# Kernel tuning notes

Measured on AMD Instinct MI355X. Metric: run time of the kernel, lower is better.

Reference implementation:

```python
import jax, jax.numpy as jnp
import numpy as np

EMBED = 1024
HEADS = 16
HEAD_DIM = EMBED // HEADS


def setup_inputs() -> dict:
    key = jax.random.key(0)
    ks = jax.random.split(key, 6)
    s = 1.0 / np.sqrt(EMBED)
    return {
        "x": jax.random.normal(ks[0], (2, 2048, EMBED), dtype=jnp.float32),
        "Wq": jax.random.normal(ks[1], (EMBED, EMBED), dtype=jnp.float32) * s,
        "Wk": jax.random.normal(ks[2], (EMBED, EMBED), dtype=jnp.float32) * s,
        "Wv": jax.random.normal(ks[3], (EMBED, EMBED), dtype=jnp.float32) * s,
        "Wfc": jax.random.normal(ks[4], (EMBED, EMBED), dtype=jnp.float32) * s,
        "bfc": jnp.zeros((EMBED,), dtype=jnp.float32),
    }


def reference(x, Wq, Wk, Wv, Wfc, bfc):
    # x: (N, L, E). Linear(E,E,bias=False) applies y = x @ W.T (torch convention).
    N, L, E = x.shape
    q = (x @ Wq.T).reshape(N, L, HEADS, HEAD_DIM)
    k = (x @ Wk.T).reshape(N, L, HEADS, HEAD_DIM)
    v = (x @ Wv.T).reshape(N, L, HEADS, HEAD_DIM)
    # energy: (N, H, Q, K)
    energy = jnp.einsum('nqhd,nkhd->nhqk', q, k)
    # NOTE: original scales by sqrt(embed_size), not sqrt(head_dim)
    attn = jax.nn.softmax(energy / jnp.sqrt(jnp.float32(E)), axis=3)
    out = jnp.einsum('nhql,nlhd->nqhd', attn, v).reshape(N, L, E)
    return out @ Wfc.T + bfc
```

## Files before the change

kernel.cpp:

```cpp
#include <hip/hip_runtime.h>
#include <stdint.h>


typedef short bf16x8 __attribute__((ext_vector_type(8)));
typedef short bf16x4 __attribute__((ext_vector_type(4)));
typedef float f32x4 __attribute__((ext_vector_type(4)));

__device__ __forceinline__ unsigned short f2bf(float f) {
  union { float f; unsigned u; } v; v.f = f;
  return (unsigned short)((v.u + 0x7FFFu + ((v.u >> 16) & 1u)) >> 16);
}

#if defined(__has_builtin)
#if __has_builtin(__builtin_amdgcn_cvt_pk_bf16_f32)
#define HAVE_PK_BF16 1
#endif
#if __has_builtin(__builtin_amdgcn_exp2f)
#define EXP2(x) __builtin_amdgcn_exp2f(x)
#endif
#endif
#ifndef EXP2
#define EXP2(x) exp2f(x)
#endif

__device__ __forceinline__ unsigned pk2bf(float a, float b) {
#ifdef HAVE_PK_BF16
  typedef __bf16 bfv2 __attribute__((ext_vector_type(2)));
  union { bfv2 v; unsigned u; } c;
  c.v = __builtin_amdgcn_cvt_pk_bf16_f32(a, b);
  return c.u;
#else
  return (unsigned)f2bf(a) | ((unsigned)f2bf(b) << 16);
#endif
}

__device__ __forceinline__ void load_lds16(const unsigned short* g, unsigned short* l) {
  __builtin_amdgcn_global_load_lds(
      (const __attribute__((address_space(1))) unsigned int*)(const void*)g,
      (__attribute__((address_space(3))) unsigned int*)(void*)l, 16, 0, 0);
}

#define MFMA16(a, b, c) __builtin_amdgcn_mfma_f32_16x16x32_bf16((a), (b), (c), 0, 0, 0)

#if defined(__has_builtin)
#if __has_builtin(__builtin_amdgcn_mfma_f32_16x16x16bf16_1k)
#define MFMAK16(a, b, c) __builtin_amdgcn_mfma_f32_16x16x16bf16_1k((a), (b), (c), 0, 0, 0)
#elif __has_builtin(__builtin_amdgcn_mfma_f32_16x16x16_bf16)
#define MFMAK16(a, b, c) __builtin_amdgcn_mfma_f32_16x16x16_bf16((a), (b), (c), 0, 0, 0)
#endif
#endif
#ifndef MFMAK16
__device__ __forceinline__ f32x4 mfmak16_asm(bf16x4 a, bf16x4 b, f32x4 c) {
  asm volatile("v_mfma_f32_16x16x16_bf16 %0, %1, %2, %0" : "+v"(c) : "v"(a), "v"(b));
  return c;
}
#define MFMAK16(a, b, c) mfmak16_asm((a), (b), (c))
#endif

__global__ __launch_bounds__(256) void cvt_all_kernel(
    const float* __restrict__ x, const float* __restrict__ w0, const float* __restrict__ w1,
    const float* __restrict__ w2, const float* __restrict__ w3, unsigned short* __restrict__ xb,
    unsigned short* __restrict__ d0, unsigned short* __restrict__ d1,
    unsigned short* __restrict__ d2, unsigned short* __restrict__ d3) {
  int i = blockIdx.x * 256 + threadIdx.x;
  const float* s;
  unsigned short* d;
  int off;
  if (i < 1048576) {
    s = x; d = xb; off = i;
  } else {
    int j = i - 1048576;
    int w = j >> 18;
    off = j & 262143;
    s = (w == 0) ? w0 : (w == 1) ? w1 : (w == 2) ? w2 : w3;
    d = (w == 0) ? d0 : (w == 1) ? d1 : (w == 2) ? d2 : d3;
  }
  float4 f = ((const float4*)s)[off];
  uint2 o;
  o.x = pk2bf(f.x, f.y);
  o.y = pk2bf(f.z, f.w);
  ((uint2*)d)[off] = o;
}

__global__ __launch_bounds__(256) void gemm_qkv_kernel(
    const unsigned short* __restrict__ Xb, const unsigned short* __restrict__ Wqb,
    const unsigned short* __restrict__ Wkb, const unsigned short* __restrict__ Wvb,
    unsigned short* __restrict__ Qo, unsigned short* __restrict__ Ko,
    unsigned short* __restrict__ Vt) {
  __shared__ __align__(16) unsigned short As[128 * 32];
  __shared__ __align__(16) unsigned short Bs[128 * 32];
  const int mode = blockIdx.z;
  const unsigned short* W = (mode == 0) ? Wqb : ((mode == 1) ? Wkb : Wvb);
  const int n0 = blockIdx.x * 128;
  const int m0 = blockIdx.y * 128;
  const int tid = threadIdx.x;
  const int lane = tid & 63;
  const int wv = tid >> 6;
  const int wm = (wv >> 1) * 64;
  const int wn = (wv & 1) * 64;
  const int qq = lane >> 4;
  const int cc = lane & 15;

  const f32x4 fz = {0.f, 0.f, 0.f, 0.f};
  f32x4 acc[4][4];
#pragma unroll
  for (int i = 0; i < 4; i++)
#pragma unroll
    for (int j = 0; j < 4; j++) acc[i][j] = fz;

  const int ia0 = tid, ia1 = tid + 256;
  const int ra0 = ia0 >> 2, ca0 = (ia0 & 3) * 8;
  const int ra1 = ia1 >> 2, ca1 = (ia1 & 3) * 8;

  for (int k0 = 0; k0 < 1024; k0 += 32) {
    __syncthreads();
    load_lds16(Xb + (m0 + ra0) * 1024 + k0 + ca0, As + ia0 * 8);
    load_lds16(Xb + (m0 + ra1) * 1024 + k0 + ca1, As + ia1 * 8);
    load_lds16(W + (n0 + ra0) * 1024 + k0 + ca0, Bs + ia0 * 8);
    load_lds16(W + (n0 + ra1) * 1024 + k0 + ca1, Bs + ia1 * 8);
    __syncthreads();
    bf16x8 a[4], b[4];
#pragma unroll
    for (int i = 0; i < 4; i++) a[i] = *(const bf16x8*)(As + (wm + i * 16 + cc) * 32 + qq * 8);
#pragma unroll
    for (int j = 0; j < 4; j++) b[j] = *(const bf16x8*)(Bs + (wn + j * 16 + cc) * 32 + qq * 8);
    if (mode < 2) {
#pragma unroll
      for (int i = 0; i < 4; i++)
#pragma unroll
        for (int j = 0; j < 4; j++) acc[i][j] = MFMA16(b[j], a[i], acc[i][j]);
    } else {
#pragma unroll
      for (int i = 0; i < 4; i++)
#pragma unroll
        for (int j = 0; j < 4; j++) acc[i][j] = MFMA16(a[i], b[j], acc[i][j]);
    }
  }

  if (mode < 2) {
    const float esc = (mode == 0) ? 0.0450842200277801f : 1.0f;
    unsigned short* dst = (mode == 0) ? Qo : Ko;
#pragma unroll
    for (int i = 0; i < 4; i++) {
      int row = m0 + wm + i * 16 + cc;
#pragma unroll
      for (int j = 0; j < 4; j++) {
        int col = n0 + wn + j * 16 + qq * 4;
        uint2 pk;
        pk.x = pk2bf(acc[i][j][0] * esc, acc[i][j][1] * esc);
        pk.y = pk2bf(acc[i][j][2] * esc, acc[i][j][3] * esc);
        *(uint2*)(dst + row * 1024 + col) = pk;
      }
    }
  } else {
#pragma unroll
    for (int i = 0; i < 4; i++)
#pragma unroll
      for (int j = 0; j < 4; j++) {
        int row = m0 + wm + i * 16 + qq * 4;
        int nn = row >> 11, ll = row & 2047;
        int col = n0 + wn + j * 16 + cc;
        int hh = col >> 6, dd = col & 63;
        uint2 pk;
        pk.x = pk2bf(acc[i][j][0], acc[i][j][1]);
        pk.y = pk2bf(acc[i][j][2], acc[i][j][3]);
        *(uint2*)(Vt + ((nn * 16 + hh) * 64 + dd) * 2048 + ll) = pk;
      }
  }
}

__global__ __launch_bounds__(256, 2) void attn_kernel(const unsigned short* __restrict__ Qg,
                                                      const unsigned short* __restrict__ Kg,
                                                      const unsigned short* __restrict__ Vg,
                                                      unsigned short* __restrict__ Og) {
  __shared__ __align__(16) unsigned short smem[2][2][8192];
  const int qt = blockIdx.x, hh = blockIdx.y, nb = blockIdx.z;
  const int tid = threadIdx.x, lane = tid & 63, wv = tid >> 6;
  const int pair = wv >> 1, wq = wv & 1;
  const int qq = lane >> 4, cc = lane & 15;
  const int q0 = qt * 128 + wq * 64;
  const unsigned short* Kbase = Kg + (size_t)(nb * 2048 + pair * 1024) * 1024 + hh * 64;
  const unsigned short* Vbase = Vg + (size_t)((nb * 16 + hh) * 64) * 2048 + pair * 1024;

  const int lr = lane >> 3;
  const int lc8 = ((lane & 7) ^ lr) * 8;
  const int ldl = lane * 8;

  bf16x8 qf[4][2];
#pragma unroll
  for (int rt = 0; rt < 4; rt++)
#pragma unroll
    for (int kc = 0; kc < 2; kc++)
      qf[rt][kc] = *(const bf16x8*)(Qg + (size_t)(nb * 2048 + q0 + rt * 16 + cc) * 1024 +
                                    hh * 64 + kc * 32 + qq * 8);

  const f32x4 fz = {0.f, 0.f, 0.f, 0.f};
  f32x4 o[4][4];
  float lsum[4] = {0.f, 0.f, 0.f, 0.f};
#pragma unroll
  for (int rt = 0; rt < 4; rt++)
#pragma unroll
    for (int vt = 0; vt < 4; vt++) o[rt][vt] = fz;

  {
    unsigned short* Kb = &smem[pair][0][0];
    unsigned short* Vb = &smem[pair][0][4096];
#pragma unroll
    for (int i = 0; i < 4; i++) {
      int CI = wq * 4 + i;
      load_lds16(Kbase + (size_t)(CI * 8 + lr) * 1024 + lc8, Kb + CI * 512 + ldl);
      load_lds16(Vbase + (size_t)(CI * 8 + lr) * 2048 + lc8, Vb + CI * 512 + ldl);
    }
  }
  __syncthreads();

#pragma unroll 1
  for (int it = 0; it < 16; it++) {
    const int buf = it & 1;
    if (it < 15) {
      const int ktn = (it + 1) * 64;
      unsigned short* Kb = &smem[pair][buf ^ 1][0];
      unsigned short* Vb = &smem[pair][buf ^ 1][4096];
#pragma unroll
      for (int i = 0; i < 4; i++) {
        int CI = wq * 4 + i;
        load_lds16(Kbase + (size_t)(ktn + CI * 8 + lr) * 1024 + lc8, Kb + CI * 512 + ldl);
        load_lds16(Vbase + (size_t)(CI * 8 + lr) * 2048 + ktn + lc8, Vb + CI * 512 + ldl);
      }
    }
    const unsigned short* Kp = &smem[pair][buf][0];
    const unsigned short* Vp = &smem[pair][buf][4096];
#pragma unroll
    for (int st = 0; st < 4; st++) {
      const unsigned short* kr = Kp + (st * 16 + cc) * 64;
      int ch0 = (qq ^ (cc & 7)) << 3;
      bf16x8 k0 = *(const bf16x8*)(kr + ch0);
      bf16x8 k1 = *(const bf16x8*)(kr + (ch0 ^ 32));
      f32x4 z[4];
#pragma unroll
      for (int rt = 0; rt < 4; rt++) {
        z[rt] = MFMA16(k0, qf[rt][0], fz);
        z[rt] = MFMA16(k1, qf[rt][1], z[rt]);
      }
      bf16x4 bp[4];
#pragma unroll
      for (int rt = 0; rt < 4; rt++) {
        float p0 = EXP2(z[rt][0]), p1 = EXP2(z[rt][1]);
        float p2 = EXP2(z[rt][2]), p3 = EXP2(z[rt][3]);
        lsum[rt] += (p0 + p1) + (p2 + p3);
        union { uint2 u; bf16x4 v; } pk;
        pk.u.x = pk2bf(p0, p1);
        pk.u.y = pk2bf(p2, p3);
        bp[rt] = pk.v;
      }
      int vc = st * 2 + (qq >> 1);
      int voff = (qq & 1) * 4;
#pragma unroll
      for (int vt = 0; vt < 4; vt++) {
        bf16x4 vf = *(const bf16x4*)(Vp + (vt * 16 + cc) * 64 + ((vc ^ (cc & 7)) << 3) + voff);
#pragma unroll
        for (int rt = 0; rt < 4; rt++) o[rt][vt] = MFMAK16(vf, bp[rt], o[rt][vt]);
      }
    }
    __syncthreads();
  }

#pragma unroll
  for (int rt = 0; rt < 4; rt++) {
    float l = lsum[rt];
    l += __shfl_xor(l, 16);
    l += __shfl_xor(l, 32);
    lsum[rt] = l;
  }

  float* oex = (float*)&smem[0][0][0];
  float* lex = oex + 8192;
  __syncthreads();
  if (pair == 1) {
#pragma unroll
    for (int rt = 0; rt < 4; rt++) {
#pragma unroll
      for (int vt = 0; vt < 4; vt++) {
        int idx = (((wq * 4 + rt) * 4 + vt) * 4 + qq) * 16 + cc;
        *(f32x4*)(oex + idx * 4) = o[rt][vt];
      }
      if (qq == 0) lex[(wq * 4 + rt) * 16 + cc] = lsum[rt];
    }
  }
  __syncthreads();
  if (pair == 0) {
#pragma unroll
    for (int rt = 0; rt < 4; rt++) {
      float rinv = 1.0f / (lsum[rt] + lex[(wq * 4 + rt) * 16 + cc]);
#pragma unroll
      for (int vt = 0; vt < 4; vt++) {
        int idx = (((wq * 4 + rt) * 4 + vt) * 4 + qq) * 16 + cc;
        f32x4 op = *(const f32x4*)(oex + idx * 4);
        uint2 ov;
        ov.x = pk2bf((o[rt][vt][0] + op[0]) * rinv, (o[rt][vt][1] + op[1]) * rinv);
        ov.y = pk2bf((o[rt][vt][2] + op[2]) * rinv, (o[rt][vt][3] + op[3]) * rinv);
        *(uint2*)(Og + (size_t)(nb * 2048 + q0 + rt * 16 + cc) * 1024 + hh * 64 + vt * 16 +
                  qq * 4) = ov;
      }
    }
  }
}

__global__ __launch_bounds__(256) void gemm_fc_kernel(const unsigned short* __restrict__ Ab,
                                                      const unsigned short* __restrict__ Wb,
                                                      const float* __restrict__ bias,
                                                      float* __restrict__ Co) {
  __shared__ __align__(16) unsigned short As[64 * 32];
  __shared__ __align__(16) unsigned short Bs[128 * 32];
  const int n0 = blockIdx.x * 128;
  const int m0 = blockIdx.y * 64;
  const int tid = threadIdx.x;
  const int lane = tid & 63;
  const int wv = tid >> 6;
  const int wm = (wv & 1) * 32;
  const int wn = (wv >> 1) * 64;
  const int qq = lane >> 4;
  const int cc = lane & 15;

  const f32x4 fz = {0.f, 0.f, 0.f, 0.f};
  f32x4 acc[2][4];
#pragma unroll
  for (int i = 0; i < 2; i++)
#pragma unroll
    for (int j = 0; j < 4; j++) acc[i][j] = fz;

  const int raA = tid >> 2, caA = (tid & 3) * 8;
  const int ia0 = tid, ia1 = tid + 256;
  const int rb0 = ia0 >> 2, cb0 = (ia0 & 3) * 8;
  const int rb1 = ia1 >> 2, cb1 = (ia1 & 3) * 8;

  for (int k0 = 0; k0 < 1024; k0 += 32) {
    __syncthreads();
    load_lds16(Ab + (m0 + raA) * 1024 + k0 + caA, As + tid * 8);
    load_lds16(Wb + (n0 + rb0) * 1024 + k0 + cb0, Bs + ia0 * 8);
    load_lds16(Wb + (n0 + rb1) * 1024 + k0 + cb1, Bs + ia1 * 8);
    __syncthreads();
    bf16x8 a[2], b[4];
#pragma unroll
    for (int i = 0; i < 2; i++) a[i] = *(const bf16x8*)(As + (wm + i * 16 + cc) * 32 + qq * 8);
#pragma unroll
    for (int j = 0; j < 4; j++) b[j] = *(const bf16x8*)(Bs + (wn + j * 16 + cc) * 32 + qq * 8);
#pragma unroll
    for (int i = 0; i < 2; i++)
#pragma unroll
      for (int j = 0; j < 4; j++) acc[i][j] = MFMA16(b[j], a[i], acc[i][j]);
  }

#pragma unroll
  for (int i = 0; i < 2; i++) {
    int row = m0 + wm + i * 16 + cc;
#pragma unroll
    for (int j = 0; j < 4; j++) {
      int col = n0 + wn + j * 16 + qq * 4;
      float4 bb = *(const float4*)(bias + col);
      float4 ov;
      ov.x = acc[i][j][0] + bb.x;
      ov.y = acc[i][j][1] + bb.y;
      ov.z = acc[i][j][2] + bb.z;
      ov.w = acc[i][j][3] + bb.w;
      *(float4*)(Co + (size_t)row * 1024 + col) = ov;
    }
  }
}

extern "C" void kernel_launch(void* const* d_in, const int* in_sizes, int n_in, void* d_out,
                              int out_size, void* d_ws, size_t ws_size, hipStream_t stream) {
  const float* x = (const float*)d_in[0];
  const float* Wq = (const float*)d_in[1];
  const float* Wk = (const float*)d_in[2];
  const float* Wv = (const float*)d_in[3];
  const float* Wfc = (const float*)d_in[4];
  const float* bfc = (const float*)d_in[5];
  float* out = (float*)d_out;
  char* ws = (char*)d_ws;
  unsigned short* xb = (unsigned short*)(ws);
  unsigned short* wqb = (unsigned short*)(ws + (8u << 20));
  unsigned short* wkb = (unsigned short*)(ws + (10u << 20));
  unsigned short* wvb = (unsigned short*)(ws + (12u << 20));
  unsigned short* wfb = (unsigned short*)(ws + (14u << 20));
  unsigned short* Qb = (unsigned short*)(ws + (16u << 20));
  unsigned short* Kb = (unsigned short*)(ws + (24u << 20));
  unsigned short* Vtb = (unsigned short*)(ws + (32u << 20));
  unsigned short* Ob = (unsigned short*)(ws + (40u << 20));

  cvt_all_kernel<<<8192, 256, 0, stream>>>(x, Wq, Wk, Wv, Wfc, xb, wqb, wkb, wvb, wfb);
  gemm_qkv_kernel<<<dim3(8, 32, 3), 256, 0, stream>>>(xb, wqb, wkb, wvb, Qb, Kb, Vtb);
  attn_kernel<<<dim3(16, 16, 2), 256, 0, stream>>>(Qb, Kb, Vtb, Ob);
  gemm_fc_kernel<<<dim3(8, 64), 256, 0, stream>>>(Ob, wfb, bfc, out);
}
```

Baseline: 200.8 us.

## Double-buffer QKV GEMM LDS tiles with K=64 steps and XOR swizzle

Restructures the QKV projection GEMM main loop to use two LDS buffers with a K-step of 64. The next tile's global-to-LDS loads are issued before computing on the current one, leaving one barrier per iteration instead of two. It also XOR-swizzles the LDS column slots to reduce bank conflicts on the 16-byte fragment reads, and adds a launch bound hint of 2 blocks per CU. LDS use grows to 64KB per block, which may limit occupancy.

```diff
diff --git a/kernel.cpp b/kernel.cpp
--- a/kernel.cpp
+++ b/kernel.cpp
@@ -82,13 +82,12 @@
   ((uint2*)d)[off] = o;
 }
 
-__global__ __launch_bounds__(256) void gemm_qkv_kernel(
+__global__ __launch_bounds__(256, 2) void gemm_qkv_kernel(
     const unsigned short* __restrict__ Xb, const unsigned short* __restrict__ Wqb,
     const unsigned short* __restrict__ Wkb, const unsigned short* __restrict__ Wvb,
     unsigned short* __restrict__ Qo, unsigned short* __restrict__ Ko,
     unsigned short* __restrict__ Vt) {
-  __shared__ __align__(16) unsigned short As[128 * 32];
-  __shared__ __align__(16) unsigned short Bs[128 * 32];
+  __shared__ __align__(16) unsigned short smem[2][16384];
   const int mode = blockIdx.z;
   const unsigned short* W = (mode == 0) ? Wqb : ((mode == 1) ? Wkb : Wvb);
   const int n0 = blockIdx.x * 128;
@@ -108,33 +107,69 @@
 #pragma unroll
     for (int j = 0; j < 4; j++) acc[i][j] = fz;
 
-  const int ia0 = tid, ia1 = tid + 256;
-  const int ra0 = ia0 >> 2, ca0 = (ia0 & 3) * 8;
-  const int ra1 = ia1 >> 2, ca1 = (ia1 & 3) * 8;
-
-  for (int k0 = 0; k0 < 1024; k0 += 32) {
+  const int srow = tid >> 3;
+  const int scol = (((tid & 7) ^ (srow & 7)) * 8);
+  const unsigned short* gA[4];
+  const unsigned short* gB[4];
+#pragma unroll
+  for (int i = 0; i < 4; i++) {
+    gA[i] = Xb + (size_t)(m0 + i * 32 + srow) * 1024 + scol;
+    gB[i] = W + (size_t)(n0 + i * 32 + srow) * 1024 + scol;
+  }
+  const int ldst = tid * 8;
+
+#pragma unroll
+  for (int i = 0; i < 4; i++) {
+    load_lds16(gA[i], smem[0] + i * 2048 + ldst);
+    load_lds16(gB[i], smem[0] + 8192 + i * 2048 + ldst);
+    gA[i] += 64;
+    gB[i] += 64;
+  }
+  __syncthreads();
+
+#pragma unroll 1
+  for (int it = 0; it < 16; it++) {
+    const int buf = it & 1;
+    if (it < 15) {
+      unsigned short* dst = smem[buf ^ 1];
+#pragma unroll
+      for (int i = 0; i < 4; i++) {
+        load_lds16(gA[i], dst + i * 2048 + ldst);
+        load_lds16(gB[i], dst + 8192 + i * 2048 + ldst);
+        gA[i] += 64;
+        gB[i] += 64;
+      }
+    }
+    const unsigned short* Ab = smem[buf];
+    const unsigned short* Bb = smem[buf] + 8192;
+#pragma unroll
+    for (int kc = 0; kc < 2; kc++) {
+      bf16x8 a[4], b[4];
+#pragma unroll
+      for (int i = 0; i < 4; i++) {
+        int row = wm + i * 16 + cc;
+        int slot = (kc * 4 + qq) ^ (cc & 7);
+        a[i] = *(const bf16x8*)(Ab + row * 64 + slot * 8);
+      }
+#pragma unroll
+      for (int j = 0; j < 4; j++) {
+        int row = wn + j * 16 + cc;
+        int slot = (kc * 4 + qq) ^ (cc & 7);
+        b[j] = *(const bf16x8*)(Bb + row * 64 + slot * 8);
+      }
+      if (mode < 2) {
+#pragma unroll
+        for (int i = 0; i < 4; i++)
+#pragma unroll
+          for (int j = 0; j < 4; j++) acc[i][j] = MFMA16(b[j], a[i], acc[i][j]);
+      } else {
+#pragma unroll
+        for (int i = 0; i < 4; i++)
+#pragma unroll
+          for (int j = 0; j < 4; j++) acc[i][j] = MFMA16(a[i], b[j], acc[i][j]);
+      }
+    }
     __syncthreads();
-    load_lds16(Xb + (m0 + ra0) * 1024 + k0 + ca0, As + ia0 * 8);
-    load_lds16(Xb + (m0 + ra1) * 1024 + k0 + ca1, As + ia1 * 8);
-    load_lds16(W + (n0 + ra0) * 1024 + k0 + ca0, Bs + ia0 * 8);
-    load_lds16(W + (n0 + ra1) * 1024 + k0 + ca1, Bs + ia1 * 8);
-    __syncthreads();
-    bf16x8 a[4], b[4];
-#pragma unroll
-    for (int i = 0; i < 4; i++) a[i] = *(const bf16x8*)(As + (wm + i * 16 + cc) * 32 + qq * 8);
-#pragma unroll
-    for (int j = 0; j < 4; j++) b[j] = *(const bf16x8*)(Bs + (wn + j * 16 + cc) * 32 + qq * 8);
-    if (mode < 2) {
-#pragma unroll
-      for (int i = 0; i < 4; i++)
-#pragma unroll
-        for (int j = 0; j < 4; j++) acc[i][j] = MFMA16(b[j], a[i], acc[i][j]);
-    } else {
-#pragma unroll
-      for (int i = 0; i < 4; i++)
-#pragma unroll
-        for (int j = 0; j < 4; j++) acc[i][j] = MFMA16(a[i], b[j], acc[i][j]);
-    }
   }
 
   if (mode < 2) {
```

Result: faster. 185.7 us (-7.6%).
